# Optimization experiments

Measured on AMD Instinct MI355X. Metric: run time of the kernel, lower is better.

The kernel has to match this reference:

```python
import jax, jax.numpy as jnp
import numpy as np

N_NODES = 50000
N_EDGES = 500000
IN_CH = 2
HID = 64
OUT_CH = 64
H1 = 4
H2 = 1
EDGE_DIM = 2


def _glorot(key, shape):
    fan_in, fan_out = shape[0], shape[1]
    lim = jnp.sqrt(6.0 / (fan_in + fan_out))
    return jax.random.uniform(key, shape, jnp.float32, -lim, lim)


def setup_inputs() -> dict:
    key = jax.random.key(0)
    ks = jax.random.split(key, 16)
    x = jax.random.uniform(ks[0], (N_NODES, IN_CH), jnp.float32)
    edge_index = jax.random.randint(ks[1], (2, N_EDGES), 0, N_NODES, dtype=jnp.int64)
    edge_attr = jax.random.uniform(ks[2], (N_EDGES, EDGE_DIM), jnp.float32)
    batch = jnp.zeros((N_NODES,), jnp.int32)
    # conv1 params (GATv2: lin_l, lin_r with bias, lin_edge no bias, att, out bias)
    W1l = _glorot(ks[3], (IN_CH, H1 * HID)); b1l = jnp.zeros((H1 * HID,), jnp.float32)
    W1r = _glorot(ks[4], (IN_CH, H1 * HID)); b1r = jnp.zeros((H1 * HID,), jnp.float32)
    W1e = _glorot(ks[5], (EDGE_DIM, H1 * HID))
    att1 = _glorot(ks[6], (H1, HID))
    bias1 = jnp.zeros((H1 * HID,), jnp.float32)
    # conv2 params
    W2l = _glorot(ks[7], (H1 * HID, H2 * OUT_CH)); b2l = jnp.zeros((H2 * OUT_CH,), jnp.float32)
    W2r = _glorot(ks[8], (H1 * HID, H2 * OUT_CH)); b2r = jnp.zeros((H2 * OUT_CH,), jnp.float32)
    W2e = _glorot(ks[9], (EDGE_DIM, H2 * OUT_CH))
    att2 = _glorot(ks[10], (H2, OUT_CH))
    bias2 = jnp.zeros((H2 * OUT_CH,), jnp.float32)
    return dict(x=x, edge_attr=edge_attr,
                W1l=W1l, b1l=b1l, W1r=W1r, b1r=b1r, W1e=W1e, att1=att1, bias1=bias1,
                W2l=W2l, b2l=b2l, W2r=W2r, b2r=b2r, W2e=W2e, att2=att2, bias2=bias2,
                edge_index=edge_index, batch=batch)


def _segment_softmax(alpha, seg, num_segments):
    # alpha: [E, H], seg: [E] destination ids
    amax = jax.ops.segment_max(alpha, seg, num_segments=num_segments)
    amax = jnp.where(jnp.isfinite(amax), amax, 0.0)
    ex = jnp.exp(alpha - amax[seg])
    denom = jax.ops.segment_sum(ex, seg, num_segments=num_segments)
    return ex / (denom[seg] + 1e-16)


def _gatv2_conv(x, edge_index, edge_attr, Wl, bl, Wr, br, We, att, bias, heads, out_c):
    N = x.shape[0]
    src, dst = edge_index[0], edge_index[1]
    # add self loops with fill_value='mean' for edge_attr (PyG default)
    ones = jnp.ones((src.shape[0],), x.dtype)
    deg = jax.ops.segment_sum(ones, dst, num_segments=N)
    loop_attr = jax.ops.segment_sum(edge_attr, dst, num_segments=N) / jnp.maximum(deg, 1.0)[:, None]
    loops = jnp.arange(N, dtype=src.dtype)
    src = jnp.concatenate([src, loops])
    dst = jnp.concatenate([dst, loops])
    ea = jnp.concatenate([edge_attr, loop_attr], axis=0)
    xl = (x @ Wl + bl).reshape(N, heads, out_c)   # source-side transform
    xr = (x @ Wr + br).reshape(N, heads, out_c)   # target-side transform
    ee = (ea @ We).reshape(-1, heads, out_c)
    e = jax.nn.leaky_relu(xl[src] + xr[dst] + ee, 0.2)   # [E', H, C]
    alpha = jnp.einsum('ehc,hc->eh', e, att)
    alpha = _segment_softmax(alpha, dst, N)
    out = jax.ops.segment_sum(xl[src] * alpha[..., None], dst, num_segments=N)
    return out.reshape(N, heads * out_c) + bias


def reference(x, edge_attr, W1l, b1l, W1r, b1r, W1e, att1, bias1,
              W2l, b2l, W2r, b2r, W2e, att2, bias2, edge_index, batch):
    h = jax.nn.elu(_gatv2_conv(x, edge_index, edge_attr, W1l, b1l, W1r, b1r, W1e, att1, bias1, H1, HID))
    # dropout skipped (eval mode)
    h = _gatv2_conv(h, edge_index, edge_attr, W2l, b2l, W2r, b2r, W2e, att2, bias2, H2, OUT_CH)
    # global_mean_pool over batch (single graph -> [1, OUT_CH])
    nb = 1
    cnt = jax.ops.segment_sum(jnp.ones((h.shape[0],), h.dtype), batch, num_segments=nb)
    pooled = jax.ops.segment_sum(h, batch, num_segments=nb) / jnp.maximum(cnt, 1.0)[:, None]
    return pooled
```

## Files before the change

kernel.cpp:

```cpp
#include <hip/hip_runtime.h>
#include <hip/hip_bf16.h>

#define N_NODES 50000
#define N_EDGES 500000
#define E_AUG   (N_EDGES + N_NODES)
#define NH1 4
#define HID 64
#define C2  64

#define NBUCK 49
#define BCAP  16384

#define NL2B    2048
#define L2CHUNK 272
#define L2BINS  320

typedef unsigned int uint32;
typedef unsigned short ushort16;
typedef __attribute__((ext_vector_type(8))) short short8v;
typedef __attribute__((ext_vector_type(4))) float f32x4;

__device__ __forceinline__ ushort16 f2bf(float f) {
    union { float f; uint32 u; } v; v.f = f;
    uint32 u = v.u + (0x7FFFu + ((v.u >> 16) & 1u));
    return (ushort16)(u >> 16);
}
__device__ __forceinline__ float bf2f(ushort16 h) {
    union { uint32 u; float f; } v; v.u = ((uint32)h) << 16;
    return v.f;
}


__global__ void zero_bcnt_kernel(int* __restrict__ bcnt) {
    if (threadIdx.x < 64) bcnt[threadIdx.x] = 0;
}


#define PACK_BLOCKS 128
#define HIST_BLOCKS ((N_EDGES / 4 + 255) / 256)

__global__ void pass1_kernel(const int* __restrict__ ei, const float* __restrict__ ea,
                             const float* __restrict__ W1l, const float* __restrict__ b1l,
                             const float* __restrict__ W1r, const float* __restrict__ b1r,
                             const float* __restrict__ W1e, const float* __restrict__ att1,
                             const float* __restrict__ bias1,
                             const float* __restrict__ W2l, const float* __restrict__ W2r,
                             float* __restrict__ Wpack, float* __restrict__ Apack,
                             float4* __restrict__ wpk4, ushort16* __restrict__ Wt,
                             int4* __restrict__ stage, int* __restrict__ bcnt) {
    const int tid = threadIdx.x;
    if (blockIdx.x < PACK_BLOCKS) {
        int t = blockIdx.x * 256 + tid;
        if (blockIdx.x == 0) {
            if (tid < 256) {
                int h = tid >> 6, hc = tid;
                float* wp = &Wpack[((tid & 63) * 4 + h) * 8];
                wp[0] = W1l[hc];       wp[1] = W1l[256 + hc];
                wp[2] = W1r[hc];       wp[3] = W1r[256 + hc];
                wp[4] = W1e[hc];       wp[5] = W1e[256 + hc];
                wp[6] = b1l[hc] + b1r[hc];
                wp[7] = 0.4f * att1[hc];
                wpk4[hc] = make_float4(W1l[hc], W1l[256 + hc], b1l[hc] + bias1[hc], 0.0f);
            }
            if (tid < 28) {
                int h = tid / 7, comp = tid % 7;
                float s = 0.0f;
                for (int c = 0; c < 64; ++c) {
                    int hc = h * 64 + c;
                    float m;
                    switch (comp) {
                        case 0: m = W1l[hc]; break;
                        case 1: m = W1l[256 + hc]; break;
                        case 2: m = W1r[hc]; break;
                        case 3: m = W1r[256 + hc]; break;
                        case 4: m = W1e[hc]; break;
                        case 5: m = W1e[256 + hc]; break;
                        default: m = b1l[hc] + b1r[hc]; break;
                    }
                    s += att1[hc] * m;
                }
                Apack[h * 8 + comp] = 0.6f * s;
            }
        }
        if (t < 128 * 256) {
            int c = t & 127, k = t >> 7;
            float w = (c < 64) ? W2l[k * 64 + c] : W2r[k * 64 + (c - 64)];
            Wt[c * 256 + k] = f2bf(w);
        }
    } else {
        __shared__ int lbc[NBUCK];
        __shared__ int lbase[NBUCK];
        if (tid < NBUCK) lbc[tid] = 0;
        __syncthreads();

        const int e0 = ((blockIdx.x - PACK_BLOCKS) * 256 + tid) * 4;
        int4 rec[4]; int bket[4], lofs[4];
        bool val[4];
        #pragma unroll
        for (int j = 0; j < 4; ++j) {
            const int e = e0 + j;
            val[j] = (e < N_EDGES);
            if (val[j]) {
                int s = ei[e], d = ei[N_EDGES + e];
                float2 a = *(const float2*)&ea[2 * e];
                rec[j].x = s; rec[j].y = d;
                rec[j].z = __float_as_int(a.x); rec[j].w = __float_as_int(a.y);
                bket[j] = d >> 10;
                lofs[j] = atomicAdd(&lbc[bket[j]], 1);
            }
        }
        __syncthreads();
        if (tid < NBUCK) lbase[tid] = lbc[tid] ? atomicAdd(&bcnt[tid], lbc[tid]) : 0;
        __syncthreads();
        #pragma unroll
        for (int j = 0; j < 4; ++j)
            if (val[j])
                stage[bket[j] * BCAP + lbase[bket[j]] + lofs[j]] = rec[j];
    }
}


__global__ void bscan_kernel(const int* __restrict__ bcnt, int* __restrict__ bbase,
                             int* __restrict__ offs) {
    __shared__ int s[64];
    int tid = threadIdx.x;
    int nodec = (tid < NBUCK) ? min(1024, N_NODES - tid * 1024) : 0;
    int v = (tid < NBUCK) ? bcnt[tid] + nodec : 0;
    s[tid] = v;
    __syncthreads();
    for (int off = 1; off < 64; off <<= 1) {
        int t = (tid >= off) ? s[tid - off] : 0;
        __syncthreads();
        s[tid] += t;
        __syncthreads();
    }
    if (tid < NBUCK) bbase[tid] = s[tid] - v;
    if (tid == 0) offs[N_NODES] = E_AUG;
}


__global__ void degk2_kernel(const int4* __restrict__ stage, const int* __restrict__ bcnt,
                             const int* __restrict__ bbase,
                             int* __restrict__ offs, int* __restrict__ cnt,
                             float* __restrict__ den,
                             int4* __restrict__ epk, int* __restrict__ e_src) {
    __shared__ int bins[1024];
    __shared__ float ls0[1024], ls1[1024];
    __shared__ int ssum[256];
    const int tid = threadIdx.x, bk = blockIdx.x;
    for (int i = tid; i < 1024; i += 256) { bins[i] = 0; ls0[i] = 0.0f; ls1[i] = 0.0f; }
    __syncthreads();
    const int n_ = bcnt[bk];
    for (int i = tid; i < n_; i += 256) {
        int4 r = stage[bk * BCAP + i];
        int li = r.y & 1023;
        atomicAdd(&bins[li], 1);
        atomicAdd(&ls0[li], __int_as_float(r.z));
        atomicAdd(&ls1[li], __int_as_float(r.w));
    }
    __syncthreads();

    const int nodebase = bk * 1024;
    int v[4], pfx[4];
    int tsum = 0;
    #pragma unroll
    for (int j = 0; j < 4; ++j) {
        int i = tid * 4 + j;
        int node = nodebase + i;
        v[j] = (node < N_NODES) ? bins[i] + 1 : 0;
        pfx[j] = tsum;
        tsum += v[j];
    }
    ssum[tid] = tsum;
    __syncthreads();
    for (int off = 1; off < 256; off <<= 1) {
        int t = (tid >= off) ? ssum[tid - off] : 0;
        __syncthreads();
        ssum[tid] += t;
        __syncthreads();
    }
    const int base = bbase[bk] + ssum[tid] - tsum;
    #pragma unroll
    for (int j = 0; j < 4; ++j) {
        int i = tid * 4 + j;
        int node = nodebase + i;
        if (node < N_NODES) {
            int o = base + pfx[j];
            offs[node] = o;
            cnt[node] = 0;
            den[node] = 0.0f;
            float dgf = (float)max(bins[i], 1);
            int4 sl;
            sl.x = node; sl.y = node;
            sl.z = __float_as_int(ls0[i] / dgf);
            sl.w = __float_as_int(ls1[i] / dgf);
            epk[o] = sl;
            e_src[o] = node;
        }
    }
}


__global__ void pass2_kernel(const int4* __restrict__ stage, const int* __restrict__ bcnt,
                             const int* __restrict__ offs, int* __restrict__ cnt,
                             int4* __restrict__ epk, int* __restrict__ e_src) {
    const int tid = threadIdx.x;
    const int bk = blockIdx.x >> 2, slice = blockIdx.x & 3;
    const int n = bcnt[bk];
    const int chunk = (n + 3) >> 2;
    const int lo = slice * chunk, hi = min(n, lo + chunk);
    for (int i = lo + tid; i < hi; i += 256) {
        int4 r = stage[bk * BCAP + i];
        int pos = offs[r.y] + 1 + atomicAdd(&cnt[r.y], 1);
        epk[pos] = r;
        e_src[pos] = r.x;
    }
}


__global__ __launch_bounds__(256) void l1_alpha_kernel(
    const float* __restrict__ x, const int4* __restrict__ epk,
    const float* __restrict__ Wpack, const float* __restrict__ Apack,
    float* __restrict__ alpha1) {
    __shared__ float sWp[2048];
    __shared__ float sA[32];
    const int tid = threadIdx.x;
    for (int i = tid; i < 2048; i += 256) sWp[i] = Wpack[i];
    if (tid < 32) sA[tid] = Apack[tid];
    __syncthreads();

    const int e0 = (blockIdx.x * 256 + tid) * 2;
    if (e0 >= E_AUG) return;

    const int4 v0 = epk[e0];
    const int4 v1 = epk[e0 + 1];

    float u0[2], u1[2], u2[2], u3[2], u4[2], u5[2];
    {
        const float2 xs0 = *(const float2*)&x[2 * v0.x];
        const float2 xd0 = *(const float2*)&x[2 * v0.y];
        const float2 xs1 = *(const float2*)&x[2 * v1.x];
        const float2 xd1 = *(const float2*)&x[2 * v1.y];
        u0[0] = xs0.x; u1[0] = xs0.y; u2[0] = xd0.x; u3[0] = xd0.y;
        u4[0] = __int_as_float(v0.z); u5[0] = __int_as_float(v0.w);
        u0[1] = xs1.x; u1[1] = xs1.y; u2[1] = xd1.x; u3[1] = xd1.y;
        u4[1] = __int_as_float(v1.z); u5[1] = __int_as_float(v1.w);
    }

    float p[4][2];
    #pragma unroll
    for (int h = 0; h < 4; ++h) {
        const float a0 = sA[h * 8], a1 = sA[h * 8 + 1], a2 = sA[h * 8 + 2],
                    a3 = sA[h * 8 + 3], a4 = sA[h * 8 + 4], a5 = sA[h * 8 + 5],
                    a6 = sA[h * 8 + 6];
        #pragma unroll
        for (int j = 0; j < 2; ++j)
            p[h][j] = fmaf(u0[j], a0, fmaf(u1[j], a1, fmaf(u2[j], a2,
                      fmaf(u3[j], a3, fmaf(u4[j], a4, fmaf(u5[j], a5, a6))))));
    }

    for (int c = 0; c < 64; ++c) {
        const float* wp = &sWp[c * 32];
        #pragma unroll
        for (int h = 0; h < 4; ++h) {
            const float4 wa = *(const float4*)&wp[h * 8];
            const float4 wb = *(const float4*)&wp[h * 8 + 4];
            #pragma unroll
            for (int j = 0; j < 2; ++j) {
                float t = fmaf(u0[j], wa.x,
                          fmaf(u1[j], wa.y,
                          fmaf(u2[j], wa.z,
                          fmaf(u3[j], wa.w,
                          fmaf(u4[j], wb.x,
                          fmaf(u5[j], wb.y, wb.z))))));
                p[h][j] = fmaf(fabsf(t), wb.w, p[h][j]);
            }
        }
    }

    #pragma unroll
    for (int h = 0; h < 4; ++h)
        *(float2*)&alpha1[(size_t)h * E_AUG + e0] =
            make_float2(__expf(p[h][0]), __expf(p[h][1]));
}


__global__ __launch_bounds__(256) void l1out_fused_kernel(
    const float* __restrict__ x, const int* __restrict__ offs,
    const int* __restrict__ e_src, const float* __restrict__ alpha1,
    const float4* __restrict__ wpk4, const ushort16* __restrict__ Wt,
    const float* __restrict__ b2l, const float* __restrict__ b2r,
    ushort16* __restrict__ xl2b, ushort16* __restrict__ xr2b) {
    __shared__ short hlds[64 * 256];
    __shared__ float4 swpk[256];
    const int tid = threadIdx.x;
    const int n0 = blockIdx.x * 64;
    const int lane = tid & 63, w = tid >> 6;

    swpk[tid] = wpk4[tid];

    const int nl = tid >> 2, head = tid & 3;
    const int node = n0 + nl;
    float S1 = 0.0f, S2 = 0.0f;
    if (node < N_NODES) {
        const int beg = offs[node], end = offs[node + 1];
        const float* ap = alpha1 + (size_t)head * E_AUG;
        float den = 0.0f, s1 = 0.0f, s2 = 0.0f;
        for (int e = beg; e < end; ++e) {
            float wt = ap[e];
            int s = e_src[e];
            float2 xs = *(const float2*)&x[2 * s];
            den += wt;
            s1 = fmaf(wt, xs.x, s1);
            s2 = fmaf(wt, xs.y, s2);
        }
        float inv = 1.0f / (den + 1e-16f);
        S1 = s1 * inv;
        S2 = s2 * inv;
    }
    __syncthreads();

    {
        const int kseg = head * 64;
        const int swz = (nl & 7) << 3;
        for (int i = 0; i < 8; ++i) {
            short8v hv;
            #pragma unroll
            for (int j = 0; j < 8; ++j) {
                float4 wv = swpk[kseg + i * 8 + j];
                float g = fmaf(wv.x, S1, fmaf(wv.y, S2, wv.z));
                g = g > 0.0f ? g : (__expf(g) - 1.0f);
                hv[j] = (short)f2bf(g);
            }
            *(short8v*)&hlds[(nl * 256 + kseg + i * 8) ^ swz] = hv;
        }
    }

    short8v bfrag[2][8];
    {
        const int bc = w * 32 + (lane & 15);
        const int k0 = (lane >> 4) * 8;
        #pragma unroll
        for (int ct = 0; ct < 2; ++ct)
            #pragma unroll
            for (int kb = 0; kb < 8; ++kb)
                bfrag[ct][kb] = *(const short8v*)&Wt[(size_t)(bc + ct * 16) * 256 + kb * 32 + k0];
    }
    __syncthreads();

    f32x4 acc[4][2];
    #pragma unroll
    for (int rt = 0; rt < 4; ++rt)
        #pragma unroll
        for (int ct = 0; ct < 2; ++ct)
            acc[rt][ct] = (f32x4){0.0f, 0.0f, 0.0f, 0.0f};

    const int arow = lane & 15, ak0 = (lane >> 4) * 8;
    #pragma unroll
    for (int rt = 0; rt < 4; ++rt) {
        const int n = rt * 16 + arow;
        const int swz = (n & 7) << 3;
        #pragma unroll
        for (int kb = 0; kb < 8; ++kb) {
            short8v a = *(const short8v*)&hlds[(n * 256 + kb * 32 + ak0) ^ swz];
            acc[rt][0] = __builtin_amdgcn_mfma_f32_16x16x32_bf16(a, bfrag[0][kb], acc[rt][0], 0, 0, 0);
            acc[rt][1] = __builtin_amdgcn_mfma_f32_16x16x32_bf16(a, bfrag[1][kb], acc[rt][1], 0, 0, 0);
        }
    }

    #pragma unroll
    for (int ct = 0; ct < 2; ++ct) {
        const int c = w * 32 + ct * 16 + (lane & 15);
        const bool isL = (c < 64);
        const int cc = isL ? c : c - 64;
        const float bias = isL ? b2l[cc] : b2r[cc];
        ushort16* dst = isL ? xl2b : xr2b;
        #pragma unroll
        for (int rt = 0; rt < 4; ++rt)
            #pragma unroll
            for (int r = 0; r < 4; ++r) {
                int nn = n0 + rt * 16 + (lane >> 4) * 4 + r;
                if (nn < N_NODES) dst[nn * 64 + cc] = f2bf(acc[rt][ct][r] + bias);
            }
    }
}


__global__ __launch_bounds__(256) void l2_logit_kernel(
    const ushort16* __restrict__ xl2b, const ushort16* __restrict__ xr2b,
    const int4* __restrict__ epk,
    const float* __restrict__ W2e, const float* __restrict__ att2,
    float* __restrict__ alpha2, float* __restrict__ den) {
    __shared__ float sWe[128], satt[64];
    __shared__ float bins[L2BINS];
    const int tid = threadIdx.x;
    if (tid < 128) sWe[tid] = W2e[tid];
    if (tid < 64) satt[tid] = att2[tid];
    for (int i = tid; i < L2BINS; i += 256) bins[i] = 0.0f;
    const int base = blockIdx.x * L2CHUNK;
    const int d_first = epk[min(base, E_AUG - 1)].y;
    __syncthreads();

    const int lane = tid & 63, w = tid >> 6;
    const int cl = lane & 15, g = lane >> 4;
    const uint32* xlp = (const uint32*)xl2b;
    const uint32* xrp = (const uint32*)xr2b;

    for (int it = 0; it < L2CHUNK / 16; ++it) {
        const int e = base + it * 16 + w * 4 + g;
        if (e < E_AUG) {
            const int4 v = epk[e];
            const float ae0 = __int_as_float(v.z), ae1 = __int_as_float(v.w);
            float acc = 0.0f;
            #pragma unroll
            for (int q = 0; q < 2; ++q) {
                const int c2 = cl + q * 16;
                const uint32 ul = xlp[v.x * 32 + c2];
                const uint32 ur = xrp[v.y * 32 + c2];
                const int c0 = 2 * c2, c1 = 2 * c2 + 1;
                float xl0 = bf2f((ushort16)(ul & 0xffff)), xl1 = bf2f((ushort16)(ul >> 16));
                float xr0 = bf2f((ushort16)(ur & 0xffff)), xr1 = bf2f((ushort16)(ur >> 16));
                float t0 = xl0 + xr0 + fmaf(ae0, sWe[c0], ae1 * sWe[64 + c0]);
                float t1 = xl1 + xr1 + fmaf(ae0, sWe[c1], ae1 * sWe[64 + c1]);
                t0 = t0 > 0.0f ? t0 : 0.2f * t0;
                t1 = t1 > 0.0f ? t1 : 0.2f * t1;
                acc = fmaf(t0, satt[c0], fmaf(t1, satt[c1], acc));
            }
            #pragma unroll
            for (int off = 8; off; off >>= 1) acc += __shfl_xor(acc, off);
            if (cl == 0) {
                float wv = __expf(acc);
                alpha2[e] = wv;
                int rel = v.y - d_first;
                if (rel < L2BINS) atomicAdd(&bins[rel], wv);
                else atomicAdd(&den[v.y], wv);
            }
        }
    }
    __syncthreads();
    for (int i = tid; i < L2BINS; i += 256) {
        float b = bins[i];
        int node = d_first + i;
        if (b != 0.0f && node < N_NODES) atomicAdd(&den[node], b);
    }
}


__global__ __launch_bounds__(256) void l2_pool_kernel(
    const ushort16* __restrict__ xl2b, const int4* __restrict__ epk,
    const float* __restrict__ alpha2, const float* __restrict__ den,
    float* __restrict__ pblock) {
    __shared__ float sp[16][64];
    const int tid = threadIdx.x;
    const int lane = tid & 63, w = tid >> 6;
    const int cl = lane & 15, g = lane >> 4;
    const int slot = w * 4 + g;
    const int base = blockIdx.x * L2CHUNK;
    const uint32* xlp = (const uint32*)xl2b;

    float a0 = 0.0f, a1 = 0.0f, a2 = 0.0f, a3 = 0.0f;
    for (int it = 0; it < L2CHUNK / 16; ++it) {
        const int e = base + it * 16 + w * 4 + g;
        if (e < E_AUG) {
            const int4 v = epk[e];
            const float coef = alpha2[e] / (den[v.y] + 1e-16f);
            const uint32 u0 = xlp[v.x * 32 + cl];
            const uint32 u1 = xlp[v.x * 32 + cl + 16];
            a0 = fmaf(coef, bf2f((ushort16)(u0 & 0xffff)), a0);
            a1 = fmaf(coef, bf2f((ushort16)(u0 >> 16)), a1);
            a2 = fmaf(coef, bf2f((ushort16)(u1 & 0xffff)), a2);
            a3 = fmaf(coef, bf2f((ushort16)(u1 >> 16)), a3);
        }
    }
    sp[slot][2 * cl] = a0;
    sp[slot][2 * cl + 1] = a1;
    sp[slot][2 * cl + 32] = a2;
    sp[slot][2 * cl + 33] = a3;
    __syncthreads();
    if (tid < 64) {
        float s = 0.0f;
        #pragma unroll
        for (int i = 0; i < 16; ++i) s += sp[i][tid];
        pblock[blockIdx.x * 64 + tid] = s;
    }
}


__global__ __launch_bounds__(256) void pool_partial_kernel(const float* __restrict__ pblock,
                                                           float* __restrict__ pfin) {
    __shared__ float s[256];
    int tid = threadIdx.x;
    int l = tid & 63, q = tid >> 6;
    float local = 0.0f;
    for (int r = blockIdx.x * 4 + q; r < NL2B; r += 64 * 4)
        local += pblock[r * 64 + l];
    s[tid] = local;
    __syncthreads();
    if (tid < 64) {
        float v = s[tid] + s[tid + 64] + s[tid + 128] + s[tid + 192];
        pfin[blockIdx.x * 64 + tid] = v;
    }
}

__global__ __launch_bounds__(256) void pool_final2_kernel(const float* __restrict__ pfin,
                                                          const float* __restrict__ bias2,
                                                          float* __restrict__ d_out) {
    __shared__ float s[256];
    int tid = threadIdx.x;
    int l = tid & 63, q = tid >> 6;
    float local = 0.0f;
    for (int r = q; r < 64; r += 4)
        local += pfin[r * 64 + l];
    s[tid] = local;
    __syncthreads();
    if (tid < 64) {
        float v = s[tid] + s[tid + 64] + s[tid + 128] + s[tid + 192];
        d_out[tid] = v * (1.0f / N_NODES) + bias2[tid];
    }
}


extern "C" void kernel_launch(void* const* d_in, const int* in_sizes, int n_in,
                              void* d_out, int out_size, void* d_ws, size_t ws_size,
                              hipStream_t stream) {
    const float* x     = (const float*)d_in[0];
    const float* eattr = (const float*)d_in[1];
    const float* W1l   = (const float*)d_in[2];
    const float* b1l   = (const float*)d_in[3];
    const float* W1r   = (const float*)d_in[4];
    const float* b1r   = (const float*)d_in[5];
    const float* W1e   = (const float*)d_in[6];
    const float* att1  = (const float*)d_in[7];
    const float* bias1 = (const float*)d_in[8];
    const float* W2l   = (const float*)d_in[9];
    const float* b2l   = (const float*)d_in[10];
    const float* W2r   = (const float*)d_in[11];
    const float* b2r   = (const float*)d_in[12];
    const float* W2e   = (const float*)d_in[13];
    const float* att2  = (const float*)d_in[14];
    const float* bias2 = (const float*)d_in[15];
    const int*   ei    = (const int*)d_in[16];
    float* out = (float*)d_out;

    char* p = (char*)d_ws;
    auto alloc = [&](size_t bytes) -> void* {
        void* r = (void*)p;
        p += (bytes + 255) & ~(size_t)255;
        return r;
    };
    int*   cnt    = (int*)alloc(N_NODES * 4);
    int*   bcnt   = (int*)alloc(256 * 4);
    int*   bbase  = (int*)alloc(256 * 4);
    int*   offs   = (int*)alloc((N_NODES + 1) * 4);
    float* den    = (float*)alloc(N_NODES * 4);
    int4*  stage  = (int4*)alloc((size_t)NBUCK * BCAP * 16);
    int4*  epk    = (int4*)alloc((size_t)E_AUG * 16);
    int*   e_src  = (int*)alloc(E_AUG * 4);
    float* alpha1 = (float*)alloc((size_t)E_AUG * 4 * 4);
    float* alpha2 = (float*)alloc((size_t)E_AUG * 4);
    float* Wpack  = (float*)alloc(256 * 8 * 4);
    float* Apack  = (float*)alloc(32 * 4);
    float4* wpk4  = (float4*)alloc(256 * 16);
    ushort16* Wt  = (ushort16*)alloc(128 * 256 * 2);
    ushort16* xl2b = (ushort16*)alloc((size_t)N_NODES * C2 * 2);
    ushort16* xr2b = (ushort16*)alloc((size_t)N_NODES * C2 * 2);
    float* pblock = (float*)alloc((size_t)NL2B * 64 * 4);
    float* pfin   = (float*)alloc((size_t)64 * 64 * 4);

    zero_bcnt_kernel<<<1, 64, 0, stream>>>(bcnt);

    pass1_kernel<<<PACK_BLOCKS + HIST_BLOCKS, 256, 0, stream>>>(
        ei, eattr, W1l, b1l, W1r, b1r, W1e, att1, bias1, W2l, W2r,
        Wpack, Apack, wpk4, Wt, stage, bcnt);

    bscan_kernel<<<1, 64, 0, stream>>>(bcnt, bbase, offs);

    degk2_kernel<<<NBUCK, 256, 0, stream>>>(stage, bcnt, bbase, offs, cnt, den, epk, e_src);

    pass2_kernel<<<NBUCK * 4, 256, 0, stream>>>(stage, bcnt, offs, cnt, epk, e_src);

    l1_alpha_kernel<<<(E_AUG / 2 + 255) / 256, 256, 0, stream>>>(x, epk, Wpack, Apack,
                                                                 alpha1);

    l1out_fused_kernel<<<(N_NODES + 63) / 64, 256, 0, stream>>>(x, offs, e_src, alpha1,
                                                                wpk4, Wt, b2l, b2r,
                                                                xl2b, xr2b);

    l2_logit_kernel<<<NL2B, 256, 0, stream>>>(xl2b, xr2b, epk, W2e, att2, alpha2, den);

    l2_pool_kernel<<<NL2B, 256, 0, stream>>>(xl2b, epk, alpha2, den, pblock);

    pool_partial_kernel<<<64, 256, 0, stream>>>(pblock, pfin);
    pool_final2_kernel<<<1, 256, 0, stream>>>(pfin, bias2, out);
}
```

Baseline: 214.8 us.

## Fuse degree scan and edge scatter into one 1024-thread bucket kernel

Merges the per-bucket degree/offset kernel and the edge scatter kernel into a single kernel with 1024 threads per bucket. Scatter positions come from a shared-memory cursor array instead of global atomics on a per-node count array, which also removes that array. The cost is only 49 blocks doing the scatter (previously 196), so less parallelism and a longer 1024-wide scan.

```diff
diff --git a/kernel.cpp b/kernel.cpp
--- a/kernel.cpp
+++ b/kernel.cpp
@@ -139,20 +139,23 @@
 }
 
 
-__global__ void degk2_kernel(const int4* __restrict__ stage, const int* __restrict__ bcnt,
-                             const int* __restrict__ bbase,
-                             int* __restrict__ offs, int* __restrict__ cnt,
-                             float* __restrict__ den,
-                             int4* __restrict__ epk, int* __restrict__ e_src) {
+__global__ __launch_bounds__(1024) void buildk_kernel(
+    const int4* __restrict__ stage, const int* __restrict__ bcnt,
+    const int* __restrict__ bbase,
+    int* __restrict__ offs, float* __restrict__ den,
+    int4* __restrict__ epk, int* __restrict__ e_src) {
     __shared__ int bins[1024];
     __shared__ float ls0[1024], ls1[1024];
-    __shared__ int ssum[256];
+    __shared__ int scan[1024];
+    __shared__ int cursor[1024];
     const int tid = threadIdx.x, bk = blockIdx.x;
-    for (int i = tid; i < 1024; i += 256) { bins[i] = 0; ls0[i] = 0.0f; ls1[i] = 0.0f; }
-    __syncthreads();
+    bins[tid] = 0; ls0[tid] = 0.0f; ls1[tid] = 0.0f;
+    __syncthreads();
+
     const int n_ = bcnt[bk];
-    for (int i = tid; i < n_; i += 256) {
-        int4 r = stage[bk * BCAP + i];
+    const int4* sb = stage + (size_t)bk * BCAP;
+    for (int i = tid; i < n_; i += 1024) {
+        int4 r = sb[i];
         int li = r.y & 1023;
         atomicAdd(&bins[li], 1);
         atomicAdd(&ls0[li], __int_as_float(r.z));
@@ -160,58 +163,34 @@
     }
     __syncthreads();
 
-    const int nodebase = bk * 1024;
-    int v[4], pfx[4];
-    int tsum = 0;
-    #pragma unroll
-    for (int j = 0; j < 4; ++j) {
-        int i = tid * 4 + j;
-        int node = nodebase + i;
-        v[j] = (node < N_NODES) ? bins[i] + 1 : 0;
-        pfx[j] = tsum;
-        tsum += v[j];
-    }
-    ssum[tid] = tsum;
-    __syncthreads();
-    for (int off = 1; off < 256; off <<= 1) {
-        int t = (tid >= off) ? ssum[tid - off] : 0;
-        __syncthreads();
-        ssum[tid] += t;
-        __syncthreads();
-    }
-    const int base = bbase[bk] + ssum[tid] - tsum;
-    #pragma unroll
-    for (int j = 0; j < 4; ++j) {
-        int i = tid * 4 + j;
-        int node = nodebase + i;
-        if (node < N_NODES) {
-            int o = base + pfx[j];
-            offs[node] = o;
-            cnt[node] = 0;
-            den[node] = 0.0f;
-            float dgf = (float)max(bins[i], 1);
-            int4 sl;
-            sl.x = node; sl.y = node;
-            sl.z = __float_as_int(ls0[i] / dgf);
-            sl.w = __float_as_int(ls1[i] / dgf);
-            epk[o] = sl;
-            e_src[o] = node;
-        }
-    }
-}
-
-
-__global__ void pass2_kernel(const int4* __restrict__ stage, const int* __restrict__ bcnt,
-                             const int* __restrict__ offs, int* __restrict__ cnt,
-                             int4* __restrict__ epk, int* __restrict__ e_src) {
-    const int tid = threadIdx.x;
-    const int bk = blockIdx.x >> 2, slice = blockIdx.x & 3;
-    const int n = bcnt[bk];
-    const int chunk = (n + 3) >> 2;
-    const int lo = slice * chunk, hi = min(n, lo + chunk);
-    for (int i = lo + tid; i < hi; i += 256) {
-        int4 r = stage[bk * BCAP + i];
-        int pos = offs[r.y] + 1 + atomicAdd(&cnt[r.y], 1);
+    const int node = bk * 1024 + tid;
+    const int v = (node < N_NODES) ? bins[tid] + 1 : 0;
+    scan[tid] = v;
+    __syncthreads();
+    for (int off = 1; off < 1024; off <<= 1) {
+        int t = (tid >= off) ? scan[tid - off] : 0;
+        __syncthreads();
+        scan[tid] += t;
+        __syncthreads();
+    }
+    const int o = bbase[bk] + scan[tid] - v;
+    if (node < N_NODES) {
+        offs[node] = o;
+        den[node] = 0.0f;
+        float dgf = (float)max(bins[tid], 1);
+        int4 sl;
+        sl.x = node; sl.y = node;
+        sl.z = __float_as_int(ls0[tid] / dgf);
+        sl.w = __float_as_int(ls1[tid] / dgf);
+        epk[o] = sl;
+        e_src[o] = node;
+    }
+    cursor[tid] = o + 1;
+    __syncthreads();
+
+    for (int i = tid; i < n_; i += 1024) {
+        int4 r = sb[i];
+        int pos = atomicAdd(&cursor[r.y & 1023], 1);
         epk[pos] = r;
         e_src[pos] = r.x;
     }
@@ -548,7 +527,6 @@
         p += (bytes + 255) & ~(size_t)255;
         return r;
     };
-    int*   cnt    = (int*)alloc(N_NODES * 4);
     int*   bcnt   = (int*)alloc(256 * 4);
     int*   bbase  = (int*)alloc(256 * 4);
     int*   offs   = (int*)alloc((N_NODES + 1) * 4);
@@ -575,9 +553,7 @@
 
     bscan_kernel<<<1, 64, 0, stream>>>(bcnt, bbase, offs);
 
-    degk2_kernel<<<NBUCK, 256, 0, stream>>>(stage, bcnt, bbase, offs, cnt, den, epk, e_src);
-
-    pass2_kernel<<<NBUCK * 4, 256, 0, stream>>>(stage, bcnt, offs, cnt, epk, e_src);
+    buildk_kernel<<<NBUCK, 1024, 0, stream>>>(stage, bcnt, bbase, offs, den, epk, e_src);
 
     l1_alpha_kernel<<<(E_AUG / 2 + 255) / 256, 256, 0, stream>>>(x, epk, Wpack, Apack,
                                                                  alpha1);
```

Result: faster. 208.9 us (-2.8%).
